# Kernel tuning notes

Measured on AMD Instinct MI355X. Metric: run time of the kernel, lower is better.

## Reference

```python
import jax, jax.numpy as jnp
import numpy as np


def setup_inputs() -> dict:
    key = jax.random.key(0)
    ks = jax.random.split(key, 8)
    C = 128
    Cq = C // 8  # 16
    x = jax.random.normal(ks[0], (4, C, 64, 64), dtype=jnp.float32)
    s = 1.0 / np.sqrt(C)
    wq = jax.random.normal(ks[1], (Cq, C), dtype=jnp.float32) * s
    bq = jnp.zeros((Cq,), dtype=jnp.float32)
    wk = jax.random.normal(ks[2], (Cq, C), dtype=jnp.float32) * s
    bk = jnp.zeros((Cq,), dtype=jnp.float32)
    wv = jax.random.normal(ks[3], (C, C), dtype=jnp.float32) * s
    bv = jnp.zeros((C,), dtype=jnp.float32)
    gamma = jnp.array([0.5], dtype=jnp.float32)
    return {"x": x, "wq": wq, "bq": bq, "wk": wk, "bk": bk,
            "wv": wv, "bv": bv, "gamma": gamma}


def reference(x, wq, bq, wk, bk, wv, bv, gamma):
    B, C, W, H = x.shape
    N = W * H
    xf = x.reshape(B, C, N)  # flatten spatial; 1x1 conv == channel matmul
    q = jnp.einsum('qc,bcn->bnq', wq, xf) + bq[None, None, :]  # B,N,Cq
    k = jnp.einsum('qc,bcn->bqn', wk, xf) + bk[None, :, None]  # B,Cq,N
    v = jnp.einsum('vc,bcn->bvn', wv, xf) + bv[None, :, None]  # B,C,N
    energy = jnp.einsum('bnq,bqm->bnm', q, k)                  # B,N,N (no scaling)
    attention = jax.nn.softmax(energy, axis=-1)
    out = jnp.einsum('bvm,bnm->bvn', v, attention)             # V @ A^T
    out = out.reshape(B, C, W, H)
    return gamma[0] * out + x
```

## Files before the change

kernel.cpp:

```cpp
#include <hip/hip_runtime.h>

#define B_    4
#define C_    128
#define CQ_   16
#define N_    4096
#define SPLIT 4
#define MPER  (N_ / SPLIT)
#define KVBLK 64
#define NT    (MPER / KVBLK)

typedef short          s16x8 __attribute__((ext_vector_type(8)));
typedef unsigned short u16x4 __attribute__((ext_vector_type(4)));
typedef unsigned int   u32x4 __attribute__((ext_vector_type(4)));
typedef float          f32x4 __attribute__((ext_vector_type(4)));
typedef unsigned short u16;
typedef unsigned int   u32;

__device__ __forceinline__ u16 f2bf(float f) {
    unsigned int u = __builtin_bit_cast(unsigned int, f);
    u += 0x7fffu + ((u >> 16) & 1u);
    return (u16)(u >> 16);
}
__device__ __forceinline__ float bf2f(u16 h) {
    unsigned int u = ((unsigned int)h) << 16;
    return __builtin_bit_cast(float, u);
}
__device__ __forceinline__ s16x8 ld8bf(const u16* p) {
    return *reinterpret_cast<const s16x8*>(p);
}
__device__ __forceinline__ u32 cvtpk_bf16(float lo, float hi) {
    u32 r;
    asm("v_cvt_pk_bf16_f32 %0, %1, %2" : "=v"(r) : "v"(lo), "v"(hi));
    return r;
}
__device__ __forceinline__ void gld_lds16(const u16* src, u16* lds) {
    __builtin_amdgcn_global_load_lds(
        (const __attribute__((address_space(1))) void*)src,
        (__attribute__((address_space(3))) void*)lds, 16, 0, 0);
}

__global__ __launch_bounds__(256) void proj_all_kernel(
    const float* __restrict__ x,
    const float* __restrict__ wq, const float* __restrict__ bq,
    const float* __restrict__ wk, const float* __restrict__ bk,
    const float* __restrict__ wv, const float* __restrict__ bv,
    u16* __restrict__ Qb, u16* __restrict__ Kb, u16* __restrict__ Vb)
{
    __shared__ float smem[12800];
    const int tid = threadIdx.x;
    const int b   = blockIdx.y;
    const int nl  = tid & 63;
    const int n   = blockIdx.x * 64 + nl;
    const int ch  = tid >> 6;
    const float* xp = x + ((size_t)b * C_) * N_ + n;

    if (blockIdx.z == 0) {
        float* wqs = smem;
        float* wks = smem + 2048;
        float (*part)[4][64][17] = (float (*)[4][64][17])(smem + 4096);
        for (int i = tid; i < CQ_ * C_; i += 256) { wqs[i] = wq[i]; wks[i] = wk[i]; }
        __syncthreads();

        float qa[CQ_], ka[CQ_];
#pragma unroll
        for (int j = 0; j < CQ_; ++j) { qa[j] = 0.f; ka[j] = 0.f; }
        const int c0 = ch * 32;
        for (int c = c0; c < c0 + 32; ++c) {
            const float xv = xp[(size_t)c * N_];
#pragma unroll
            for (int j = 0; j < CQ_; ++j) {
                qa[j] = fmaf(wqs[j * C_ + c], xv, qa[j]);
                ka[j] = fmaf(wks[j * C_ + c], xv, ka[j]);
            }
        }
#pragma unroll
        for (int j = 0; j < CQ_; ++j) { part[0][ch][nl][j] = qa[j]; part[1][ch][nl][j] = ka[j]; }
        __syncthreads();

        if (tid < 128) {
            const int which = tid >> 6;
            const int n2 = tid & 63;
            const float* bias = which ? bk : bq;
            alignas(16) u16 row[32];
#pragma unroll
            for (int j = 0; j < CQ_; ++j) {
                float v = part[which][0][n2][j] + part[which][1][n2][j]
                        + part[which][2][n2][j] + part[which][3][n2][j] + bias[j];
                u16 h = f2bf(v);
                row[j]       = h;
                row[CQ_ + j] = f2bf(v - bf2f(h));
            }
            u16* dst = (which ? Kb : Qb) + ((size_t)(b * N_ + blockIdx.x * 64 + n2)) * 32;
#pragma unroll
            for (int i = 0; i < 4; ++i)
                reinterpret_cast<uint4*>(dst)[i] = reinterpret_cast<const uint4*>(row)[i];
        }
    } else {
        const int cv0 = (blockIdx.z - 1) * 32;
        float* wvs = smem;
        float (*part)[64][33] = (float (*)[64][33])(smem + 4096);
        for (int i = tid; i < 32 * C_; i += 256) wvs[i] = wv[cv0 * C_ + i];
        __syncthreads();

        float acc[32];
#pragma unroll
        for (int j = 0; j < 32; ++j) acc[j] = 0.f;
        const int c0 = ch * 32;
        for (int c = c0; c < c0 + 32; ++c) {
            const float xv = xp[(size_t)c * N_];
#pragma unroll
            for (int j = 0; j < 32; ++j) acc[j] = fmaf(wvs[j * C_ + c], xv, acc[j]);
        }
#pragma unroll
        for (int j = 0; j < 32; ++j) part[ch][nl][j] = acc[j];
        __syncthreads();

        const int jq = tid >> 6;
#pragma unroll
        for (int jj = 0; jj < 8; ++jj) {
            const int j = jq * 8 + jj;
            float v = part[0][nl][j] + part[1][nl][j] + part[2][nl][j] + part[3][nl][j]
                    + bv[cv0 + j];
            Vb[((size_t)(b * C_ + cv0 + j)) * N_ + blockIdx.x * 64 + nl] = f2bf(v);
        }
    }
}

__global__ __launch_bounds__(256, 2) void attn_split_kernel(
    const u16* __restrict__ Qb, const u16* __restrict__ Kb, const u16* __restrict__ Vb,
    u16* __restrict__ Opart, float* __restrict__ Lpart)
{
    __shared__ __align__(16) u16 Kt[2][KVBLK * 32];
    __shared__ __align__(16) u16 Vt[2][C_ * KVBLK];

    const int tid  = threadIdx.x;
    const int lane = tid & 63;
    const int l16  = lane & 15;
    const int g    = lane >> 4;
    const int wave = tid >> 6;
    const int b    = blockIdx.y;
    const int n0   = blockIdx.x * 128;
    const int s    = blockIdx.z;
    const int ms   = s * MPER;

    const int qn = n0 + wave * 32 + l16;
    const s16x8 qf0 = ld8bf(Qb + ((size_t)(b * N_ + qn)) * 32 + 8 * g);
    const s16x8 qf1 = ld8bf(Qb + ((size_t)(b * N_ + qn + 16)) * 32 + 8 * g);

    const int kv_s   = tid >> 2;
    const int kcol_s = ((tid & 3) * 16) ^ ((kv_s & 3) << 4);
    const u16* ksrc0 = Kb + ((size_t)b * N_ + kv_s) * 32 + (kcol_s >> 1);
    const int vc_s   = tid >> 3;
    const u16* vsrc0[4];
#pragma unroll
    for (int i = 0; i < 4; ++i) {
        const int c_i  = i * 32 + vc_s;
        const int vcol = ((tid & 7) * 16) ^ ((c_i & 7) << 4);
        vsrc0[i] = Vb + ((size_t)(b * C_ + c_i)) * N_ + (vcol >> 1);
    }

    const int kswz  = (l16 & 3) << 4;
    const int vswz  = (l16 & 7) << 4;
    const int koff1 = l16 * 32 + (((16 * (g & 1)) ^ kswz) >> 1);
    const int koff2 = l16 * 32 + (((32 + 16 * g) ^ kswz) >> 1);
    const int voffA = l16 * 64 + (((16 * g) ^ vswz) >> 1);
    const int voffB = l16 * 64 + (((64 + 16 * g) ^ vswz) >> 1);

    const bool hig = (g >= 2);
    const bool mid = (g == 1) || (g == 2);

    f32x4 acc0[8], acc1[8];
#pragma unroll
    for (int cg = 0; cg < 8; ++cg) { acc0[cg] = {}; acc1[cg] = {}; }
    float lp0 = 0.f, lp1 = 0.f;

    auto relayout = [&](const float (&p)[4][4], int ss) -> s16x8 {
        const u32 a0 = cvtpk_bf16(p[2 * ss][0],     p[2 * ss][1]);
        const u32 b0 = cvtpk_bf16(p[2 * ss][2],     p[2 * ss][3]);
        const u32 a1 = cvtpk_bf16(p[2 * ss + 1][0], p[2 * ss + 1][1]);
        const u32 b1 = cvtpk_bf16(p[2 * ss + 1][2], p[2 * ss + 1][3]);
        const u32 mA = (u32)__shfl_xor((int)(hig ? a0 : a1), 32);
        const u32 mB = (u32)__shfl_xor((int)(hig ? b0 : b1), 32);
        const u32 oA = hig ? a1 : a0;
        const u32 oB = hig ? b1 : b0;
        const u32 eA = mid ? mA : oA;
        const u32 eB = mid ? mB : oB;
        const u32 vA = mid ? oA : mA;
        const u32 vB = mid ? oB : mB;
        const u32 xA = (u32)__shfl_xor((int)vA, 16);
        const u32 xB = (u32)__shfl_xor((int)vB, 16);
        u32x4 w;
        w[0] = (g & 1) ? xA : eA;
        w[1] = (g & 1) ? xB : eB;
        w[2] = (g & 1) ? eA : xA;
        w[3] = (g & 1) ? eB : xB;
        return __builtin_bit_cast(s16x8, w);
    };

    auto body = [&](int t, int buf) {
        if (t + 1 < NT) {
            const int mn = ms + (t + 1) * KVBLK;
            gld_lds16(ksrc0 + (size_t)mn * 32, &Kt[buf ^ 1][wave * 512]);
#pragma unroll
            for (int i = 0; i < 4; ++i)
                gld_lds16(vsrc0[i] + mn, &Vt[buf ^ 1][i * 2048 + wave * 512]);
        }
        const u16* ktb = &Kt[buf][0];
        const u16* vtb = &Vt[buf][0];

        f32x4 s0[4], s1[4];
        __builtin_amdgcn_s_setprio(1);
#pragma unroll
        for (int mg = 0; mg < 4; ++mg) {
            const s16x8 kf1 = ld8bf(ktb + koff1 + mg * 512);
            s16x8 kf2 = {};
            if (g < 2) kf2 = ld8bf(ktb + koff2 + mg * 512);
            f32x4 z0 = {}, z1 = {};
            z0 = __builtin_amdgcn_mfma_f32_16x16x32_bf16(kf1, qf0, z0, 0, 0, 0);
            z0 = __builtin_amdgcn_mfma_f32_16x16x32_bf16(kf2, qf0, z0, 0, 0, 0);
            z1 = __builtin_amdgcn_mfma_f32_16x16x32_bf16(kf1, qf1, z1, 0, 0, 0);
            z1 = __builtin_amdgcn_mfma_f32_16x16x32_bf16(kf2, qf1, z1, 0, 0, 0);
            s0[mg] = z0; s1[mg] = z1;
        }
        __builtin_amdgcn_s_setprio(0);

        s16x8 pf00, pf01, pf10, pf11;
        {
            float p[4][4];
#pragma unroll
            for (int mg = 0; mg < 4; ++mg)
#pragma unroll
                for (int i = 0; i < 4; ++i) { p[mg][i] = __expf(s0[mg][i]); lp0 += p[mg][i]; }
            pf00 = relayout(p, 0); pf01 = relayout(p, 1);
        }
        {
            float p[4][4];
#pragma unroll
            for (int mg = 0; mg < 4; ++mg)
#pragma unroll
                for (int i = 0; i < 4; ++i) { p[mg][i] = __expf(s1[mg][i]); lp1 += p[mg][i]; }
            pf10 = relayout(p, 0); pf11 = relayout(p, 1);
        }

        __builtin_amdgcn_s_setprio(1);
#pragma unroll
        for (int cg = 0; cg < 8; ++cg) {
            const s16x8 vfa = ld8bf(vtb + voffA + cg * 1024);
            acc0[cg] = __builtin_amdgcn_mfma_f32_16x16x32_bf16(vfa, pf00, acc0[cg], 0, 0, 0);
            acc1[cg] = __builtin_amdgcn_mfma_f32_16x16x32_bf16(vfa, pf10, acc1[cg], 0, 0, 0);
            const s16x8 vfb = ld8bf(vtb + voffB + cg * 1024);
            acc0[cg] = __builtin_amdgcn_mfma_f32_16x16x32_bf16(vfb, pf01, acc0[cg], 0, 0, 0);
            acc1[cg] = __builtin_amdgcn_mfma_f32_16x16x32_bf16(vfb, pf11, acc1[cg], 0, 0, 0);
        }
        __builtin_amdgcn_s_setprio(0);

        asm volatile("s_waitcnt vmcnt(0)" ::: "memory");
        __syncthreads();
    };

    gld_lds16(ksrc0 + (size_t)ms * 32, &Kt[0][wave * 512]);
#pragma unroll
    for (int i = 0; i < 4; ++i)
        gld_lds16(vsrc0[i] + ms, &Vt[0][i * 2048 + wave * 512]);
    asm volatile("s_waitcnt vmcnt(0)" ::: "memory");
    __syncthreads();

    for (int tt = 0; tt < NT / 2; ++tt) {
        body(2 * tt, 0);
        body(2 * tt + 1, 1);
    }

    lp0 += __shfl_xor(lp0, 16);  lp0 += __shfl_xor(lp0, 32);
    lp1 += __shfl_xor(lp1, 16);  lp1 += __shfl_xor(lp1, 32);
    const size_t sb = (size_t)(s * B_ + b);
    if (lane < 16) {
        Lpart[sb * N_ + n0 + wave * 32 + l16]      = lp0;
        Lpart[sb * N_ + n0 + wave * 32 + 16 + l16] = lp1;
    }

    const int na = n0 + wave * 32 + l16;
#pragma unroll
    for (int cg = 0; cg < 8; ++cg) {
#pragma unroll
        for (int i = 0; i < 4; ++i) {
            const int c = 16 * cg + 4 * g + i;
            Opart[(sb * C_ + c) * N_ + na]      = f2bf(acc0[cg][i]);
            Opart[(sb * C_ + c) * N_ + na + 16] = f2bf(acc1[cg][i]);
        }
    }
}

__global__ __launch_bounds__(256) void reduce_kernel(
    const u16* __restrict__ Opart, const float* __restrict__ Lpart,
    const float* __restrict__ x, const float* __restrict__ gamma,
    float* __restrict__ out)
{
    const int t  = blockIdx.x * 256 + threadIdx.x;
    const size_t e0 = (size_t)t * 4;
    const int n = (int)(e0 & (N_ - 1));
    const int c = (int)((e0 >> 12) & (C_ - 1));
    const int b = (int)(e0 >> 19);

    float o0 = 0.f, o1 = 0.f, o2 = 0.f, o3 = 0.f;
    f32x4 l = {};
#pragma unroll
    for (int s = 0; s < SPLIT; ++s) {
        const size_t sb = (size_t)(s * B_ + b);
        const u16x4 ov = *reinterpret_cast<const u16x4*>(Opart + (sb * C_ + c) * N_ + n);
        const f32x4 lv = *reinterpret_cast<const f32x4*>(Lpart + sb * N_ + n);
        o0 += bf2f(ov[0]); o1 += bf2f(ov[1]); o2 += bf2f(ov[2]); o3 += bf2f(ov[3]);
        l += lv;
    }
    const float gm = gamma[0];
    const f32x4 xv = *reinterpret_cast<const f32x4*>(x + e0);
    f32x4 r;
    r[0] = gm * o0 / l[0] + xv[0];
    r[1] = gm * o1 / l[1] + xv[1];
    r[2] = gm * o2 / l[2] + xv[2];
    r[3] = gm * o3 / l[3] + xv[3];
    *reinterpret_cast<f32x4*>(out + e0) = r;
}

extern "C" void kernel_launch(void* const* d_in, const int* in_sizes, int n_in,
                              void* d_out, int out_size, void* d_ws, size_t ws_size,
                              hipStream_t stream)
{
    const float* x     = (const float*)d_in[0];
    const float* wq    = (const float*)d_in[1];
    const float* bq    = (const float*)d_in[2];
    const float* wk    = (const float*)d_in[3];
    const float* bk    = (const float*)d_in[4];
    const float* wv    = (const float*)d_in[5];
    const float* bv    = (const float*)d_in[6];
    const float* gamma = (const float*)d_in[7];
    float* out = (float*)d_out;

    u16* Qb = (u16*)d_ws;
    u16* Kb = Qb + (size_t)B_ * N_ * 32;
    u16* Vb = Kb + (size_t)B_ * N_ * 32;
    u16* Opart = Vb + (size_t)B_ * C_ * N_;
    float* Lpart = (float*)(Opart + (size_t)SPLIT * B_ * C_ * N_);

    proj_all_kernel<<<dim3(N_ / 64, B_, 5), 256, 0, stream>>>(
        x, wq, bq, wk, bk, wv, bv, Qb, Kb, Vb);
    attn_split_kernel<<<dim3(N_ / 128, B_, SPLIT), 256, 0, stream>>>(
        Qb, Kb, Vb, Opart, Lpart);
    reduce_kernel<<<(B_ * C_ * N_ / 4) / 256, 256, 0, stream>>>(
        Opart, Lpart, x, gamma, out);
}
```

Before: 74.65 us.

## Use 512-thread attention blocks, MFMA row-sum, and log2e-prescaled Q

The attention kernel now runs 8 waves per block, each owning 16 query rows instead of 32. This halves the per-wave accumulators and lets more waves share the same K/V tile loads. The softmax row sum is computed with an MFMA against a vector of ones instead of scalar adds and shuffles. Q is pre-scaled by log2(e) in the projection so the kernel can use exp2f in place of __expf. The trade-off is more waves contending for the block barrier, and row sums now accumulate from bf16-rounded probabilities.

```diff
diff --git a/kernel.cpp b/kernel.cpp
--- a/kernel.cpp
+++ b/kernel.cpp
@@ -81,11 +81,12 @@
             const int which = tid >> 6;
             const int n2 = tid & 63;
             const float* bias = which ? bk : bq;
+            const float scale = which ? 1.0f : 1.4426950408889634f;
             alignas(16) u16 row[32];
 #pragma unroll
             for (int j = 0; j < CQ_; ++j) {
-                float v = part[which][0][n2][j] + part[which][1][n2][j]
-                        + part[which][2][n2][j] + part[which][3][n2][j] + bias[j];
+                float v = (part[which][0][n2][j] + part[which][1][n2][j]
+                         + part[which][2][n2][j] + part[which][3][n2][j] + bias[j]) * scale;
                 u16 h = f2bf(v);
                 row[j]       = h;
                 row[CQ_ + j] = f2bf(v - bf2f(h));
@@ -126,7 +127,7 @@
     }
 }
 
-__global__ __launch_bounds__(256, 2) void attn_split_kernel(
+__global__ __launch_bounds__(512, 4) void attn_split_kernel(
     const u16* __restrict__ Qb, const u16* __restrict__ Kb, const u16* __restrict__ Vb,
     u16* __restrict__ Opart, float* __restrict__ Lpart)
 {
@@ -143,21 +144,17 @@
     const int s    = blockIdx.z;
     const int ms   = s * MPER;
 
-    const int qn = n0 + wave * 32 + l16;
-    const s16x8 qf0 = ld8bf(Qb + ((size_t)(b * N_ + qn)) * 32 + 8 * g);
-    const s16x8 qf1 = ld8bf(Qb + ((size_t)(b * N_ + qn + 16)) * 32 + 8 * g);
+    const int qn = n0 + wave * 16 + l16;
+    const s16x8 qf = ld8bf(Qb + ((size_t)(b * N_ + qn)) * 32 + 8 * g);
 
     const int kv_s   = tid >> 2;
     const int kcol_s = ((tid & 3) * 16) ^ ((kv_s & 3) << 4);
     const u16* ksrc0 = Kb + ((size_t)b * N_ + kv_s) * 32 + (kcol_s >> 1);
-    const int vc_s   = tid >> 3;
-    const u16* vsrc0[4];
-#pragma unroll
-    for (int i = 0; i < 4; ++i) {
-        const int c_i  = i * 32 + vc_s;
-        const int vcol = ((tid & 7) * 16) ^ ((c_i & 7) << 4);
-        vsrc0[i] = Vb + ((size_t)(b * C_ + c_i)) * N_ + (vcol >> 1);
-    }
+    const int vc_s  = tid >> 3;
+    const int vcol  = ((tid & 7) * 16) ^ ((vc_s & 7) << 4);
+    const u16* vsrcA = Vb + ((size_t)(b * C_ + vc_s)) * N_ + (vcol >> 1);
+    const u16* vsrcB = Vb + ((size_t)(b * C_ + 64 + vc_s)) * N_ + (vcol >> 1);
+    const int wvb = wave * 512;
 
     const int kswz  = (l16 & 3) << 4;
     const int vswz  = (l16 & 7) << 4;
@@ -169,10 +166,13 @@
     const bool hig = (g >= 2);
     const bool mid = (g == 1) || (g == 2);
 
-    f32x4 acc0[8], acc1[8];
-#pragma unroll
-    for (int cg = 0; cg < 8; ++cg) { acc0[cg] = {}; acc1[cg] = {}; }
-    float lp0 = 0.f, lp1 = 0.f;
+    const s16x8 ones = { 0x3F80, 0x3F80, 0x3F80, 0x3F80,
+                         0x3F80, 0x3F80, 0x3F80, 0x3F80 };
+
+    f32x4 acc[8];
+#pragma unroll
+    for (int cg = 0; cg < 8; ++cg) acc[cg] = {};
+    f32x4 accl = {};
 
     auto relayout = [&](const float (&p)[4][4], int ss) -> s16x8 {
         const u32 a0 = cvtpk_bf16(p[2 * ss][0],     p[2 * ss][1]);
@@ -200,57 +200,46 @@
     auto body = [&](int t, int buf) {
         if (t + 1 < NT) {
             const int mn = ms + (t + 1) * KVBLK;
-            gld_lds16(ksrc0 + (size_t)mn * 32, &Kt[buf ^ 1][wave * 512]);
-#pragma unroll
-            for (int i = 0; i < 4; ++i)
-                gld_lds16(vsrc0[i] + mn, &Vt[buf ^ 1][i * 2048 + wave * 512]);
+            if (tid < 256) gld_lds16(ksrc0 + (size_t)mn * 32, &Kt[buf ^ 1][wvb]);
+            gld_lds16(vsrcA + mn, &Vt[buf ^ 1][wvb]);
+            gld_lds16(vsrcB + mn, &Vt[buf ^ 1][4096 + wvb]);
         }
         const u16* ktb = &Kt[buf][0];
         const u16* vtb = &Vt[buf][0];
 
-        f32x4 s0[4], s1[4];
+        f32x4 sacc[4];
         __builtin_amdgcn_s_setprio(1);
 #pragma unroll
         for (int mg = 0; mg < 4; ++mg) {
             const s16x8 kf1 = ld8bf(ktb + koff1 + mg * 512);
             s16x8 kf2 = {};
             if (g < 2) kf2 = ld8bf(ktb + koff2 + mg * 512);
-            f32x4 z0 = {}, z1 = {};
-            z0 = __builtin_amdgcn_mfma_f32_16x16x32_bf16(kf1, qf0, z0, 0, 0, 0);
-            z0 = __builtin_amdgcn_mfma_f32_16x16x32_bf16(kf2, qf0, z0, 0, 0, 0);
-            z1 = __builtin_amdgcn_mfma_f32_16x16x32_bf16(kf1, qf1, z1, 0, 0, 0);
-            z1 = __builtin_amdgcn_mfma_f32_16x16x32_bf16(kf2, qf1, z1, 0, 0, 0);
-            s0[mg] = z0; s1[mg] = z1;
+            f32x4 z = {};
+            z = __builtin_amdgcn_mfma_f32_16x16x32_bf16(kf1, qf, z, 0, 0, 0);
+            z = __builtin_amdgcn_mfma_f32_16x16x32_bf16(kf2, qf, z, 0, 0, 0);
+            sacc[mg] = z;
         }
         __builtin_amdgcn_s_setprio(0);
 
-        s16x8 pf00, pf01, pf10, pf11;
-        {
-            float p[4][4];
-#pragma unroll
-            for (int mg = 0; mg < 4; ++mg)
-#pragma unroll
-                for (int i = 0; i < 4; ++i) { p[mg][i] = __expf(s0[mg][i]); lp0 += p[mg][i]; }
-            pf00 = relayout(p, 0); pf01 = relayout(p, 1);
-        }
-        {
-            float p[4][4];
-#pragma unroll
-            for (int mg = 0; mg < 4; ++mg)
-#pragma unroll
-                for (int i = 0; i < 4; ++i) { p[mg][i] = __expf(s1[mg][i]); lp1 += p[mg][i]; }
-            pf10 = relayout(p, 0); pf11 = relayout(p, 1);
-        }
+        float p[4][4];
+#pragma unroll
+        for (int mg = 0; mg < 4; ++mg)
+#pragma unroll
+            for (int i = 0; i < 4; ++i)
+                p[mg][i] = exp2f(sacc[mg][i]);
+
+        const s16x8 pf0 = relayout(p, 0);
+        const s16x8 pf1 = relayout(p, 1);
 
         __builtin_amdgcn_s_setprio(1);
+        accl = __builtin_amdgcn_mfma_f32_16x16x32_bf16(ones, pf0, accl, 0, 0, 0);
+        accl = __builtin_amdgcn_mfma_f32_16x16x32_bf16(ones, pf1, accl, 0, 0, 0);
 #pragma unroll
         for (int cg = 0; cg < 8; ++cg) {
             const s16x8 vfa = ld8bf(vtb + voffA + cg * 1024);
-            acc0[cg] = __builtin_amdgcn_mfma_f32_16x16x32_bf16(vfa, pf00, acc0[cg], 0, 0, 0);
-            acc1[cg] = __builtin_amdgcn_mfma_f32_16x16x32_bf16(vfa, pf10, acc1[cg], 0, 0, 0);
+            acc[cg] = __builtin_amdgcn_mfma_f32_16x16x32_bf16(vfa, pf0, acc[cg], 0, 0, 0);
             const s16x8 vfb = ld8bf(vtb + voffB + cg * 1024);
-            acc0[cg] = __builtin_amdgcn_mfma_f32_16x16x32_bf16(vfb, pf01, acc0[cg], 0, 0, 0);
-            acc1[cg] = __builtin_amdgcn_mfma_f32_16x16x32_bf16(vfb, pf11, acc1[cg], 0, 0, 0);
+            acc[cg] = __builtin_amdgcn_mfma_f32_16x16x32_bf16(vfb, pf1, acc[cg], 0, 0, 0);
         }
         __builtin_amdgcn_s_setprio(0);
 
@@ -258,10 +247,9 @@
         __syncthreads();
     };
 
-    gld_lds16(ksrc0 + (size_t)ms * 32, &Kt[0][wave * 512]);
-#pragma unroll
-    for (int i = 0; i < 4; ++i)
-        gld_lds16(vsrc0[i] + ms, &Vt[0][i * 2048 + wave * 512]);
+    if (tid < 256) gld_lds16(ksrc0 + (size_t)ms * 32, &Kt[0][wvb]);
+    gld_lds16(vsrcA + ms, &Vt[0][wvb]);
+    gld_lds16(vsrcB + ms, &Vt[0][4096 + wvb]);
     asm volatile("s_waitcnt vmcnt(0)" ::: "memory");
     __syncthreads();
 
@@ -270,22 +258,16 @@
         body(2 * tt + 1, 1);
     }
 
-    lp0 += __shfl_xor(lp0, 16);  lp0 += __shfl_xor(lp0, 32);
-    lp1 += __shfl_xor(lp1, 16);  lp1 += __shfl_xor(lp1, 32);
     const size_t sb = (size_t)(s * B_ + b);
-    if (lane < 16) {
-        Lpart[sb * N_ + n0 + wave * 32 + l16]      = lp0;
-        Lpart[sb * N_ + n0 + wave * 32 + 16 + l16] = lp1;
-    }
-
-    const int na = n0 + wave * 32 + l16;
+    if (lane < 16) Lpart[sb * N_ + n0 + wave * 16 + l16] = accl[0];
+
+    const int na = n0 + wave * 16 + l16;
 #pragma unroll
     for (int cg = 0; cg < 8; ++cg) {
 #pragma unroll
         for (int i = 0; i < 4; ++i) {
             const int c = 16 * cg + 4 * g + i;
-            Opart[(sb * C_ + c) * N_ + na]      = f2bf(acc0[cg][i]);
-            Opart[(sb * C_ + c) * N_ + na + 16] = f2bf(acc1[cg][i]);
+            Opart[(sb * C_ + c) * N_ + na] = f2bf(acc[cg][i]);
         }
     }
 }
@@ -343,7 +325,7 @@
 
     proj_all_kernel<<<dim3(N_ / 64, B_, 5), 256, 0, stream>>>(
         x, wq, bq, wk, bk, wv, bv, Qb, Kb, Vb);
-    attn_split_kernel<<<dim3(N_ / 128, B_, SPLIT), 256, 0, stream>>>(
+    attn_split_kernel<<<dim3(N_ / 128, B_, SPLIT), 512, 0, stream>>>(
         Qb, Kb, Vb, Opart, Lpart);
     reduce_kernel<<<(B_ * C_ * N_ / 4) / 256, 256, 0, stream>>>(
         Opart, Lpart, x, gamma, out);
```

New measurement: 78.88 us. 5.7% more time.
